# Performance work log

Measured on AMD Instinct MI355X. Metric: run time of the kernel, lower is better.

## Reference

```python
import jax, jax.numpy as jnp
import numpy as np

O, T, DIN, H, DOUT = 50000, 500000, 128, 256, 128


def setup_inputs() -> dict:
    key = jax.random.key(0)
    ks = jax.random.split(key, 12)
    s = 0.05
    return {
        "obj_vecs": jax.random.normal(ks[0], (O, DIN), jnp.float32),
        "pred_vecs": jax.random.normal(ks[1], (T, DIN), jnp.float32),
        "edges": jax.random.randint(ks[2], (T, 2), 0, O, jnp.int64),
        "w1a": jax.random.normal(ks[3], (3 * DIN, H), jnp.float32) * s,
        "b1a": jax.random.normal(ks[4], (H,), jnp.float32) * s,
        "w1b": jax.random.normal(ks[5], (H, 2 * H + DOUT), jnp.float32) * s,
        "b1b": jax.random.normal(ks[6], (2 * H + DOUT,), jnp.float32) * s,
        "w2a": jax.random.normal(ks[7], (H, H), jnp.float32) * s,
        "b2a": jax.random.normal(ks[8], (H,), jnp.float32) * s,
        "w2b": jax.random.normal(ks[9], (H, DOUT), jnp.float32) * s,
        "b2b": jax.random.normal(ks[10], (DOUT,), jnp.float32) * s,
    }


def reference(obj_vecs, pred_vecs, edges, w1a, b1a, w1b, b1b, w2a, b2a, w2b, b2b):
    n_obj = obj_vecs.shape[0]
    h_dim = w2a.shape[0]
    d_out = w2b.shape[1]
    s_idx = edges[:, 0]
    o_idx = edges[:, 1]
    # gather subject/object node features, concat with predicate: [T, 3*Din]
    cur_t = jnp.concatenate([obj_vecs[s_idx], pred_vecs, obj_vecs[o_idx]], axis=1)
    # edge MLP (net1): Linear-ReLU-Linear-ReLU -> [T, 2H + Dout]
    new_t = jax.nn.relu(jax.nn.relu(cur_t @ w1a + b1a) @ w1b + b1b)
    new_s = new_t[:, :h_dim]
    new_p = new_t[:, h_dim:h_dim + d_out]
    new_o = new_t[:, h_dim + d_out:]
    # scatter-add pooling back to nodes, both endpoints
    idx = jnp.concatenate([s_idx, o_idx])
    vals = jnp.concatenate([new_s, new_o], axis=0)
    pooled = jax.ops.segment_sum(vals, idx, num_segments=n_obj)
    # avg pooling: divide by per-node incidence count (clamped to >= 1)
    counts = jax.ops.segment_sum(jnp.ones(idx.shape[0], obj_vecs.dtype), idx,
                                 num_segments=n_obj)
    pooled = pooled / jnp.clip(counts, 1.0)[:, None]
    # node MLP (net2)
    new_obj = jax.nn.relu(jax.nn.relu(pooled @ w2a + b2a) @ w2b + b2b)
    return new_obj, new_p
```

## Files before the change

kernel.cpp:

```cpp
#include <hip/hip_runtime.h>


using f32x4 = __attribute__((ext_vector_type(4))) float;
using s16x8 = __attribute__((ext_vector_type(8))) short;
typedef unsigned short u16x8 __attribute__((ext_vector_type(8)));

static __device__ __forceinline__ unsigned short f2b(float f) {
    unsigned int u = __float_as_uint(f);
    unsigned int r = (u + 0x7fffu + ((u >> 16) & 1u)) >> 16;
    return (unsigned short)r;
}

static __device__ __forceinline__ float b2f(unsigned short b) {
    return __uint_as_float(((unsigned)b) << 16);
}

static __device__ __forceinline__ unsigned swz(unsigned row, unsigned byteoff) {
    return byteoff ^ ((row & 7u) << 4);
}

static __device__ __forceinline__ void gload_lds16(const unsigned short* g, unsigned short* l) {
    __builtin_amdgcn_global_load_lds(
        (const __attribute__((address_space(1))) unsigned int*)g,
        (__attribute__((address_space(3))) unsigned int*)l,
        16, 0, 0);
}

__global__ void prep_weights(const float* __restrict__ w1a, const float* __restrict__ w1b,
                             const float* __restrict__ w2a, const float* __restrict__ w2b,
                             unsigned short* __restrict__ w1aT, unsigned short* __restrict__ w1bT,
                             unsigned short* __restrict__ w2aT, unsigned short* __restrict__ w2bT) {
    int t = blockIdx.x * blockDim.x + threadIdx.x;
    if (t < 6 * 16384) {
        int kt = t >> 14;
        int rem = t & 16383; int c = rem >> 6, kk = rem & 63;
        unsigned byte = ((unsigned)(c * 128 + kk * 2)) ^ ((c & 7u) << 4);
        *(unsigned short*)((char*)w1aT + (size_t)kt * 32768 + byte) =
            f2b(w1a[(size_t)(kt * 64 + kk) * 256 + c]);
        return;
    }
    t -= 98304;
    if (t < 10 * 16384) {
        int tile = t >> 14; int nc = tile >> 1, kh = tile & 1;
        int rem = t & 16383; int c = rem >> 7, kk = rem & 127;
        unsigned byte = ((unsigned)(c * 256 + kk * 2)) ^ ((c & 7u) << 4);
        *(unsigned short*)((char*)w1bT + (size_t)tile * 32768 + byte) =
            f2b(w1b[(size_t)(kh * 128 + kk) * 640 + nc * 128 + c]);
        return;
    }
    t -= 163840;
    if (t < 65536) { int n = t >> 8, k = t & 255; w2aT[t] = f2b(w2a[k * 256 + n]); return; }
    t -= 65536;
    if (t < 32768) { int n = t >> 8, k = t & 255; w2bT[t] = f2b(w2b[k * 128 + n]); return; }
}

__global__ void count_kernel_i(const int* __restrict__ edges, int* __restrict__ cnt, int T) {
    int e = blockIdx.x * blockDim.x + threadIdx.x;
    if (e < T) {
        atomicAdd(&cnt[edges[2 * (long long)e]], 1);
        atomicAdd(&cnt[edges[2 * (long long)e + 1]], 1);
    }
}

__global__ void scan_kernel(const int* __restrict__ cnt, int* __restrict__ rowptr,
                            int* __restrict__ cursor, int O) {
    __shared__ int sc[1024];
    const int tid = threadIdx.x;
    const int per = (O + 1023) >> 10;
    const int base = tid * per;
    int s = 0;
    for (int i = 0; i < per; ++i) { int j = base + i; if (j < O) s += cnt[j]; }
    sc[tid] = s;
    __syncthreads();
    for (int d = 1; d < 1024; d <<= 1) {
        int v = (tid >= d) ? sc[tid - d] : 0;
        __syncthreads();
        sc[tid] += v;
        __syncthreads();
    }
    int off = sc[tid] - s;
    for (int i = 0; i < per; ++i) {
        int j = base + i;
        if (j < O) { rowptr[j] = off; cursor[j] = off; off += cnt[j]; }
    }
    if (tid == 0) rowptr[O] = sc[1023];
}

__global__ void fill_kernel(const int* __restrict__ edges, int* __restrict__ cursor,
                            int* __restrict__ csr, int T) {
    int e = blockIdx.x * blockDim.x + threadIdx.x;
    if (e < T) {
        int s = edges[2 * (long long)e];
        int o = edges[2 * (long long)e + 1];
        int ps = atomicAdd(&cursor[s], 1); csr[ps] = e;
        int po = atomicAdd(&cursor[o], 1); csr[po] = T + e;
    }
}

__global__ __launch_bounds__(512, 2) void edge_mlp(
    const float* __restrict__ obj, const float* __restrict__ pred,
    const int* __restrict__ edges,
    const unsigned short* __restrict__ w1aT, const float* __restrict__ b1a,
    const unsigned short* __restrict__ w1bT, const float* __restrict__ b1b,
    unsigned short* __restrict__ edgeout, float* __restrict__ outP, int T) {
    const int m0 = blockIdx.x * 128;
    const int tid = threadIdx.x;
    const int lane = tid & 63, wid = tid >> 6;
    const int wm = wid >> 2, wn = wid & 3;
    const bool evenL = ((lane & 1) == 0);

    __shared__ unsigned short U[65536];
    char* const ldsb = (char*)U;
    unsigned short* const abuf0 = (unsigned short*)(ldsb);
    unsigned short* const abuf1 = (unsigned short*)(ldsb + 16384);
    unsigned short* const Hbuf  = (unsigned short*)(ldsb);
    unsigned short* const bbuf0 = (unsigned short*)(ldsb + 65536);
    unsigned short* const bbuf1 = (unsigned short*)(ldsb + 98304);

    bool okR[4][4];
    #pragma unroll
    for (int mi = 0; mi < 4; ++mi)
        #pragma unroll
        for (int rr = 0; rr < 4; ++rr)
            okR[mi][rr] = (m0 + wm * 64 + mi * 16 + ((lane >> 4) << 2) + rr) < T;

    const int r = tid >> 2;
    const int q = tid & 3;
    int e_r = m0 + r; if (e_r >= T) e_r = T - 1;
    const int sIdx_r = edges[2 * (long long)e_r];
    const int oIdx_r = edges[2 * (long long)e_r + 1];

    auto aSrc = [&](int kt) -> const float4* {
        const float* s;
        if (kt < 2)      s = obj  + (long long)sIdx_r * 128 + kt * 64;
        else if (kt < 4) s = pred + (long long)e_r   * 128 + (kt - 2) * 64;
        else             s = obj  + (long long)oIdx_r * 128 + (kt - 4) * 64;
        return (const float4*)s;
    };

    auto stageB = [&](const unsigned short* gt, unsigned short* bb) {
        #pragma unroll
        for (int rr4 = 0; rr4 < 4; ++rr4) {
            unsigned off = wid * 4096u + rr4 * 1024u;
            gload_lds16((const unsigned short*)((const char*)gt + off + lane * 16u),
                        (unsigned short*)((char*)bb + off));
        }
    };

    auto writeA = [&](const float4* ap, unsigned short* ab) {
        #pragma unroll
        for (int i = 0; i < 4; ++i) {
            float4 v = ap[i];
            ushort4 pk; pk.x = f2b(v.x); pk.y = f2b(v.y); pk.z = f2b(v.z); pk.w = f2b(v.w);
            unsigned byte = (r * 128u + q * 32u + i * 8u) ^ ((r & 7u) << 4);
            *(ushort4*)((char*)ab + byte) = pk;
        }
    };

    f32x4 acc1[4][4];
    #pragma unroll
    for (int a = 0; a < 4; ++a)
        #pragma unroll
        for (int b = 0; b < 4; ++b) acc1[a][b] = f32x4{0.f, 0.f, 0.f, 0.f};

    auto mfma1 = [&](const unsigned short* ab, const unsigned short* bb) {
        #pragma unroll
        for (int ks = 0; ks < 2; ++ks) {
            const unsigned kk = ks * 32u + ((lane >> 4) << 3);
            s16x8 af[4];
            #pragma unroll
            for (int mi = 0; mi < 4; ++mi) {
                unsigned row = wm * 64u + mi * 16u + (lane & 15);
                af[mi] = *(const s16x8*)((const char*)ab + ((row * 128u + kk * 2u) ^ ((row & 7u) << 4)));
            }
            #pragma unroll
            for (int nj = 0; nj < 4; ++nj) {
                unsigned c = wn * 64u + nj * 16u + (lane & 15);
                s16x8 bf = *(const s16x8*)((const char*)bb + ((c * 128u + kk * 2u) ^ ((c & 7u) << 4)));
                #pragma unroll
                for (int mi = 0; mi < 4; ++mi)
                    acc1[mi][nj] = __builtin_amdgcn_mfma_f32_16x16x32_bf16(af[mi], bf, acc1[mi][nj], 0, 0, 0);
            }
        }
    };

    float4 ap[4];
    {
        const float4* s4 = aSrc(0);
        #pragma unroll
        for (int i = 0; i < 4; ++i) ap[i] = s4[q * 4 + i];
    }
    stageB(w1aT, bbuf0);
    writeA(ap, abuf0);
    __syncthreads();

    #pragma unroll
    for (int kt = 0; kt < 6; ++kt) {
        if (kt < 5) {
            const float4* s4 = aSrc(kt + 1);
            #pragma unroll
            for (int i = 0; i < 4; ++i) ap[i] = s4[q * 4 + i];
            stageB(w1aT + (size_t)(kt + 1) * 16384, ((kt + 1) & 1) ? bbuf1 : bbuf0);
        }
        mfma1((kt & 1) ? abuf1 : abuf0, (kt & 1) ? bbuf1 : bbuf0);
        if (kt < 5) writeA(ap, ((kt + 1) & 1) ? abuf1 : abuf0);
        __syncthreads();
    }

    stageB(w1bT, bbuf0);
    #pragma unroll
    for (int nj = 0; nj < 4; ++nj) {
        int col = wn * 64 + nj * 16 + (lane & 15);
        float bias = b1a[col];
        #pragma unroll
        for (int mi = 0; mi < 4; ++mi)
            #pragma unroll
            for (int rr = 0; rr < 4; ++rr) {
                unsigned row = wm * 64u + mi * 16u + ((lane >> 4) << 2) + rr;
                float v = acc1[mi][nj][rr] + bias;
                v = v > 0.f ? v : 0.f;
                *(unsigned short*)((char*)Hbuf + swz(row, row * 512u + col * 2u)) = f2b(v);
            }
    }
    __syncthreads();

    #pragma unroll
    for (int nc = 0; nc < 5; ++nc) {
        f32x4 acc2[4][2];
        #pragma unroll
        for (int a = 0; a < 4; ++a)
            #pragma unroll
            for (int b = 0; b < 2; ++b) acc2[a][b] = f32x4{0.f, 0.f, 0.f, 0.f};

        #pragma unroll
        for (int kh = 0; kh < 2; ++kh) {
            const int t10 = nc * 2 + kh;
            if (t10 < 9) stageB(w1bT + (size_t)(t10 + 1) * 16384, ((t10 + 1) & 1) ? bbuf1 : bbuf0);
            const unsigned short* bb = (t10 & 1) ? bbuf1 : bbuf0;
            #pragma unroll
            for (int ks = 0; ks < 4; ++ks) {
                const unsigned kkB = ks * 32u + ((lane >> 4) << 3);
                const unsigned kkH = kh * 128u + kkB;
                s16x8 af[4];
                #pragma unroll
                for (int mi = 0; mi < 4; ++mi) {
                    unsigned row = wm * 64u + mi * 16u + (lane & 15);
                    af[mi] = *(const s16x8*)((const char*)Hbuf + swz(row, row * 512u + kkH * 2u));
                }
                #pragma unroll
                for (int nj = 0; nj < 2; ++nj) {
                    unsigned c = wn * 32u + nj * 16u + (lane & 15);
                    s16x8 bf = *(const s16x8*)((const char*)bb + ((c * 256u + kkB * 2u) ^ ((c & 7u) << 4)));
                    #pragma unroll
                    for (int mi = 0; mi < 4; ++mi)
                        acc2[mi][nj] = __builtin_amdgcn_mfma_f32_16x16x32_bf16(af[mi], bf, acc2[mi][nj], 0, 0, 0);
                }
            }
            __syncthreads();
        }

        if (nc == 2) {
            #pragma unroll
            for (int nj = 0; nj < 2; ++nj) {
                int col = nc * 128 + wn * 32 + nj * 16 + (lane & 15);
                float bias = b1b[col];
                #pragma unroll
                for (int mi = 0; mi < 4; ++mi)
                    #pragma unroll
                    for (int rr = 0; rr < 4; ++rr) {
                        int row = wm * 64 + mi * 16 + ((lane >> 4) << 2) + rr;
                        if (okR[mi][rr]) {
                            float v = acc2[mi][nj][rr] + bias;
                            v = v > 0.f ? v : 0.f;
                            outP[(long long)(m0 + row) * 128 + (col - 256)] = v;
                        }
                    }
            }
        } else {
            #pragma unroll
            for (int nj = 0; nj < 2; ++nj) {
                int col = nc * 128 + wn * 32 + nj * 16 + (lane & 15);
                float bias = b1b[col];
                int pc = (nc < 2) ? col : (col - 384);
                int pcb = (lane & 1) ? (pc - 1) : pc;
                #pragma unroll
                for (int mi = 0; mi < 4; ++mi) {
                    float vv[4];
                    #pragma unroll
                    for (int rr = 0; rr < 4; ++rr) {
                        float v = acc2[mi][nj][rr] + bias;
                        vv[rr] = v > 0.f ? v : 0.f;
                    }
                    float nb0 = __shfl_xor(vv[0], 1);
                    float nb1 = __shfl_xor(vv[1], 1);
                    float nb2 = __shfl_xor(vv[2], 1);
                    float nb3 = __shfl_xor(vv[3], 1);
                    #pragma unroll
                    for (int k = 0; k < 2; ++k) {
                        float lo = evenL ? (k ? vv[1] : vv[0]) : (k ? nb3 : nb2);
                        float hi = evenL ? (k ? nb1 : nb0) : (k ? vv[3] : vv[2]);
                        int rsel = evenL ? k : 2 + k;
                        if (okR[mi][rsel]) {
                            int row = wm * 64 + mi * 16 + ((lane >> 4) << 2) + rsel;
                            size_t e = (size_t)(m0 + row);
                            size_t rid = (nc < 2) ? e : (size_t)T + e;
                            unsigned pk = ((unsigned)f2b(hi) << 16) | f2b(lo);
                            *(unsigned*)(edgeout + rid * 256 + pcb) = pk;
                        }
                    }
                }
            }
        }
    }
}

__global__ __launch_bounds__(256, 4) void pool_gather(
    const unsigned short* __restrict__ edgeout, const int* __restrict__ rowptr,
    const int* __restrict__ csr, unsigned short* __restrict__ pooled, int O) {
    int w = blockIdx.x * 4 + (threadIdx.x >> 6);
    if (w >= O) return;
    const int lane = threadIdx.x & 63;
    const int beg = rowptr[w], end = rowptr[w + 1];
    float ax = 0.f, ay = 0.f, az = 0.f, aw = 0.f;
    float bx = 0.f, by = 0.f, bz = 0.f, bw = 0.f;
    int i = beg;
    for (; i + 1 < end; i += 2) {
        int r0 = csr[i], r1 = csr[i + 1];
        ushort4 v0 = *(const ushort4*)(edgeout + (size_t)r0 * 256 + lane * 4);
        ushort4 v1 = *(const ushort4*)(edgeout + (size_t)r1 * 256 + lane * 4);
        ax += b2f(v0.x); ay += b2f(v0.y); az += b2f(v0.z); aw += b2f(v0.w);
        bx += b2f(v1.x); by += b2f(v1.y); bz += b2f(v1.z); bw += b2f(v1.w);
    }
    if (i < end) {
        int r0 = csr[i];
        ushort4 v0 = *(const ushort4*)(edgeout + (size_t)r0 * 256 + lane * 4);
        ax += b2f(v0.x); ay += b2f(v0.y); az += b2f(v0.z); aw += b2f(v0.w);
    }
    float inv = 1.f / fmaxf((float)(end - beg), 1.f);
    ushort4 o4;
    o4.x = f2b((ax + bx) * inv); o4.y = f2b((ay + by) * inv);
    o4.z = f2b((az + bz) * inv); o4.w = f2b((aw + bw) * inv);
    *(ushort4*)(pooled + (size_t)w * 256 + lane * 4) = o4;
}

__global__ __launch_bounds__(256, 2) void obj_mlp(
    const unsigned short* __restrict__ pooled,
    const unsigned short* __restrict__ w2aT, const float* __restrict__ b2a,
    const unsigned short* __restrict__ w2bT, const float* __restrict__ b2b,
    float* __restrict__ outObj, int O) {
    const int m0 = blockIdx.x * 64;
    const int tid = threadIdx.x;
    const int lane = tid & 63, wid = tid >> 6;
    const int wm = wid >> 1, wn = wid & 1;

    __shared__ unsigned short Abuf[64 * 256];

    {
        const int r = tid >> 2, q = tid & 3;
        int objc = m0 + r; if (objc >= O) objc = O - 1;
        const u16x8* s8 = (const u16x8*)(pooled + (size_t)objc * 256);
        #pragma unroll
        for (int i = 0; i < 8; ++i) {
            u16x8 v = s8[q * 8 + i];
            unsigned byte = r * 512u + (q * 64u + i * 8u) * 2u;
            *(u16x8*)((char*)Abuf + swz(r, byte)) = v;
        }
    }
    __syncthreads();

    f32x4 acc1[2][2][4];
    #pragma unroll
    for (int a = 0; a < 2; ++a)
        #pragma unroll
        for (int b = 0; b < 2; ++b)
            #pragma unroll
            for (int c = 0; c < 4; ++c) acc1[a][b][c] = f32x4{0.f, 0.f, 0.f, 0.f};
    #pragma unroll
    for (int ks = 0; ks < 8; ++ks) {
        const int klane = ks * 32 + ((lane >> 4) << 3);
        s16x8 af[2];
        #pragma unroll
        for (int mi = 0; mi < 2; ++mi) {
            int row = wm * 32 + mi * 16 + (lane & 15);
            af[mi] = *(const s16x8*)((const char*)Abuf + swz(row, row * 512u + klane * 2u));
        }
        #pragma unroll
        for (int nb = 0; nb < 2; ++nb)
            #pragma unroll
            for (int nj = 0; nj < 4; ++nj) {
                int col = nb * 128 + wn * 64 + nj * 16 + (lane & 15);
                s16x8 bf = *(const s16x8*)(w2aT + (long long)col * 256 + klane);
                #pragma unroll
                for (int mi = 0; mi < 2; ++mi)
                    acc1[nb][mi][nj] = __builtin_amdgcn_mfma_f32_16x16x32_bf16(af[mi], bf, acc1[nb][mi][nj], 0, 0, 0);
            }
    }
    __syncthreads();

    #pragma unroll
    for (int nb = 0; nb < 2; ++nb)
        #pragma unroll
        for (int nj = 0; nj < 4; ++nj) {
            int col = nb * 128 + wn * 64 + nj * 16 + (lane & 15);
            float bias = b2a[col];
            #pragma unroll
            for (int mi = 0; mi < 2; ++mi)
                #pragma unroll
                for (int rr = 0; rr < 4; ++rr) {
                    int row = wm * 32 + mi * 16 + ((lane >> 4) << 2) + rr;
                    float v = acc1[nb][mi][nj][rr] + bias;
                    v = v > 0.f ? v : 0.f;
                    *(unsigned short*)((char*)Abuf + swz(row, row * 512u + col * 2u)) = f2b(v);
                }
        }
    __syncthreads();

    f32x4 acc2[2][4];
    #pragma unroll
    for (int b = 0; b < 2; ++b)
        #pragma unroll
        for (int c = 0; c < 4; ++c) acc2[b][c] = f32x4{0.f, 0.f, 0.f, 0.f};
    #pragma unroll
    for (int ks = 0; ks < 8; ++ks) {
        const int klane = ks * 32 + ((lane >> 4) << 3);
        s16x8 af[2];
        #pragma unroll
        for (int mi = 0; mi < 2; ++mi) {
            int row = wm * 32 + mi * 16 + (lane & 15);
            af[mi] = *(const s16x8*)((const char*)Abuf + swz(row, row * 512u + klane * 2u));
        }
        #pragma unroll
        for (int nj = 0; nj < 4; ++nj) {
            int col = wn * 64 + nj * 16 + (lane & 15);
            s16x8 bf = *(const s16x8*)(w2bT + (long long)col * 256 + klane);
            #pragma unroll
            for (int mi = 0; mi < 2; ++mi)
                acc2[mi][nj] = __builtin_amdgcn_mfma_f32_16x16x32_bf16(af[mi], bf, acc2[mi][nj], 0, 0, 0);
        }
    }

    #pragma unroll
    for (int nj = 0; nj < 4; ++nj) {
        int col = wn * 64 + nj * 16 + (lane & 15);
        float bias = b2b[col];
        #pragma unroll
        for (int mi = 0; mi < 2; ++mi)
            #pragma unroll
            for (int rr = 0; rr < 4; ++rr) {
                int row = wm * 32 + mi * 16 + ((lane >> 4) << 2) + rr;
                int o = m0 + row;
                if (o < O) {
                    float v = acc2[mi][nj][rr] + bias;
                    v = v > 0.f ? v : 0.f;
                    outObj[(long long)o * 128 + col] = v;
                }
            }
    }
}

extern "C" void kernel_launch(void* const* d_in, const int* in_sizes, int n_in,
                              void* d_out, int out_size, void* d_ws, size_t ws_size,
                              hipStream_t stream) {
    const float* obj  = (const float*)d_in[0];
    const float* pred = (const float*)d_in[1];
    const int*   edges = (const int*)d_in[2];
    const float* w1a = (const float*)d_in[3];
    const float* b1a = (const float*)d_in[4];
    const float* w1b = (const float*)d_in[5];
    const float* b1b = (const float*)d_in[6];
    const float* w2a = (const float*)d_in[7];
    const float* b2a = (const float*)d_in[8];
    const float* w2b = (const float*)d_in[9];
    const float* b2b = (const float*)d_in[10];

    const int O = in_sizes[0] / 128;
    const int T = in_sizes[1] / 128;

    auto al = [](size_t x) { return (x + 255) & ~(size_t)255; };
    const size_t szEdgeout = (size_t)2 * T * 256 * 2;
    const size_t szPooled  = (size_t)O * 256 * 2;
    const size_t szCnt     = (size_t)O * 4;
    const size_t szRow     = (size_t)(O + 1) * 4;
    const size_t szCsr     = (size_t)2 * T * 4;

    size_t off = 0;
    char* ws = (char*)d_ws;
    unsigned short* edgeout = (unsigned short*)(ws + off); off += al(szEdgeout);
    unsigned short* pooled  = (unsigned short*)(ws + off); off += al(szPooled);
    int* cnt    = (int*)(ws + off); off += al(szCnt);
    int* cursor = (int*)(ws + off); off += al(szCnt);
    int* rowptr = (int*)(ws + off); off += al(szRow);
    int* csr    = (int*)(ws + off); off += al(szCsr);
    unsigned short* w1aT = (unsigned short*)(ws + off); off += (size_t)6 * 16384 * 2;
    unsigned short* w1bT = (unsigned short*)(ws + off); off += (size_t)10 * 16384 * 2;
    unsigned short* w2aT = (unsigned short*)(ws + off); off += (size_t)256 * 256 * 2;
    unsigned short* w2bT = (unsigned short*)(ws + off);

    float* outObj = (float*)d_out;
    float* outP   = (float*)d_out + (size_t)O * 128;

    hipMemsetAsync(cnt, 0, szCnt, stream);
    const int prepElems = 98304 + 163840 + 65536 + 32768;
    prep_weights<<<(prepElems + 255) / 256, 256, 0, stream>>>(w1a, w1b, w2a, w2b, w1aT, w1bT, w2aT, w2bT);
    count_kernel_i<<<(T + 255) / 256, 256, 0, stream>>>(edges, cnt, T);
    scan_kernel<<<1, 1024, 0, stream>>>(cnt, rowptr, cursor, O);
    fill_kernel<<<(T + 255) / 256, 256, 0, stream>>>(edges, cursor, csr, T);
    edge_mlp<<<(T + 127) / 128, 512, 0, stream>>>(obj, pred, edges, w1aT, b1a, w1bT, b1b, edgeout, outP, T);
    pool_gather<<<(O + 3) / 4, 256, 0, stream>>>(edgeout, rowptr, csr, pooled, O);
    obj_mlp<<<(O + 63) / 64, 256, 0, stream>>>(pooled, w2aT, b2a, w2bT, b2b, outObj, O);
}
```

Before: 1.003 ms.

## Replace syncthreads with fine-grained waitcnt barriers and deepen prefetch in edge MLP

Replaces __syncthreads in the fused edge MLP with explicit vmcnt/lgkmcnt waits and raw barriers. A-tile gathers are now issued two stages ahead, and the first w1b tile is prefetched during the last GEMM1 step. It also preloads biases into registers, raises wave priority around MFMA sections, and unrolls the pooling gather by four to keep more loads in flight. Hand-tuned vmcnt counts must match the compiler's actual outstanding memory ops; if they do not, this risks races or correctness bugs.

```diff
diff --git a/kernel.cpp b/kernel.cpp
--- a/kernel.cpp
+++ b/kernel.cpp
@@ -4,6 +4,14 @@
 using f32x4 = __attribute__((ext_vector_type(4))) float;
 using s16x8 = __attribute__((ext_vector_type(8))) short;
 typedef unsigned short u16x8 __attribute__((ext_vector_type(8)));
+
+#define VMCNT0  asm volatile("s_waitcnt vmcnt(0)" ::: "memory")
+#define VMCNT4  asm volatile("s_waitcnt vmcnt(4)" ::: "memory")
+#define VMCNT16 asm volatile("s_waitcnt vmcnt(16)" ::: "memory")
+#define VMCNT32 asm volatile("s_waitcnt vmcnt(32)" ::: "memory")
+#define LGKM0   asm volatile("s_waitcnt lgkmcnt(0)" ::: "memory")
+#define BAR     __builtin_amdgcn_s_barrier()
+#define SCHEDB  __builtin_amdgcn_sched_barrier(0)
 
 static __device__ __forceinline__ unsigned short f2b(float f) {
     unsigned int u = __float_as_uint(f);
@@ -130,6 +138,15 @@
     const int sIdx_r = edges[2 * (long long)e_r];
     const int oIdx_r = edges[2 * (long long)e_r + 1];
 
+    float bias1[4], bias2[5][2];
+    #pragma unroll
+    for (int nj = 0; nj < 4; ++nj) bias1[nj] = b1a[wn * 64 + nj * 16 + (lane & 15)];
+    #pragma unroll
+    for (int nc = 0; nc < 5; ++nc)
+        #pragma unroll
+        for (int nj = 0; nj < 2; ++nj)
+            bias2[nc][nj] = b1b[nc * 128 + wn * 32 + nj * 16 + (lane & 15)];
+
     auto aSrc = [&](int kt) -> const float4* {
         const float* s;
         if (kt < 2)      s = obj  + (long long)sIdx_r * 128 + kt * 64;
@@ -190,39 +207,58 @@
         #pragma unroll
         for (int i = 0; i < 4; ++i) ap[i] = s4[q * 4 + i];
     }
+    writeA(ap, abuf0);
     stageB(w1aT, bbuf0);
-    writeA(ap, abuf0);
-    __syncthreads();
+    {
+        const float4* s4 = aSrc(1);
+        #pragma unroll
+        for (int i = 0; i < 4; ++i) ap[i] = s4[q * 4 + i];
+    }
+    VMCNT4;
+    LGKM0;
+    BAR; SCHEDB;
 
     #pragma unroll
     for (int kt = 0; kt < 6; ++kt) {
+        if (kt < 5) stageB(w1aT + (size_t)(kt + 1) * 16384, ((kt + 1) & 1) ? bbuf1 : bbuf0);
+        else        stageB(w1bT, bbuf0);
+        __builtin_amdgcn_s_setprio(1);
+        mfma1((kt & 1) ? abuf1 : abuf0, (kt & 1) ? bbuf1 : bbuf0);
+        __builtin_amdgcn_s_setprio(0);
         if (kt < 5) {
-            const float4* s4 = aSrc(kt + 1);
-            #pragma unroll
-            for (int i = 0; i < 4; ++i) ap[i] = s4[q * 4 + i];
-            stageB(w1aT + (size_t)(kt + 1) * 16384, ((kt + 1) & 1) ? bbuf1 : bbuf0);
-        }
-        mfma1((kt & 1) ? abuf1 : abuf0, (kt & 1) ? bbuf1 : bbuf0);
-        if (kt < 5) writeA(ap, ((kt + 1) & 1) ? abuf1 : abuf0);
-        __syncthreads();
-    }
-
-    stageB(w1bT, bbuf0);
+            VMCNT4;
+            writeA(ap, ((kt + 1) & 1) ? abuf1 : abuf0);
+            if (kt < 4) {
+                const float4* s4 = aSrc(kt + 2);
+                #pragma unroll
+                for (int i = 0; i < 4; ++i) ap[i] = s4[q * 4 + i];
+                VMCNT4;
+            } else {
+                VMCNT0;
+            }
+            LGKM0;
+            BAR; SCHEDB;
+        }
+    }
+
+    LGKM0;
+    BAR; SCHEDB;
     #pragma unroll
     for (int nj = 0; nj < 4; ++nj) {
-        int col = wn * 64 + nj * 16 + (lane & 15);
-        float bias = b1a[col];
         #pragma unroll
         for (int mi = 0; mi < 4; ++mi)
             #pragma unroll
             for (int rr = 0; rr < 4; ++rr) {
                 unsigned row = wm * 64u + mi * 16u + ((lane >> 4) << 2) + rr;
-                float v = acc1[mi][nj][rr] + bias;
+                unsigned col = wn * 64u + nj * 16u + (lane & 15);
+                float v = acc1[mi][nj][rr] + bias1[nj];
                 v = v > 0.f ? v : 0.f;
                 *(unsigned short*)((char*)Hbuf + swz(row, row * 512u + col * 2u)) = f2b(v);
             }
     }
-    __syncthreads();
+    LGKM0;
+    VMCNT0;
+    BAR; SCHEDB;
 
     #pragma unroll
     for (int nc = 0; nc < 5; ++nc) {
@@ -237,6 +273,7 @@
             const int t10 = nc * 2 + kh;
             if (t10 < 9) stageB(w1bT + (size_t)(t10 + 1) * 16384, ((t10 + 1) & 1) ? bbuf1 : bbuf0);
             const unsigned short* bb = (t10 & 1) ? bbuf1 : bbuf0;
+            __builtin_amdgcn_s_setprio(1);
             #pragma unroll
             for (int ks = 0; ks < 4; ++ks) {
                 const unsigned kkB = ks * 32u + ((lane >> 4) << 3);
@@ -256,31 +293,36 @@
                         acc2[mi][nj] = __builtin_amdgcn_mfma_f32_16x16x32_bf16(af[mi], bf, acc2[mi][nj], 0, 0, 0);
                 }
             }
-            __syncthreads();
+            __builtin_amdgcn_s_setprio(0);
+
+            if (kh == 0) {
+                VMCNT0;
+                BAR; SCHEDB;
+            }
         }
 
         if (nc == 2) {
             #pragma unroll
             for (int nj = 0; nj < 2; ++nj) {
                 int col = nc * 128 + wn * 32 + nj * 16 + (lane & 15);
-                float bias = b1b[col];
                 #pragma unroll
                 for (int mi = 0; mi < 4; ++mi)
                     #pragma unroll
                     for (int rr = 0; rr < 4; ++rr) {
                         int row = wm * 64 + mi * 16 + ((lane >> 4) << 2) + rr;
                         if (okR[mi][rr]) {
-                            float v = acc2[mi][nj][rr] + bias;
+                            float v = acc2[mi][nj][rr] + bias2[nc][nj];
                             v = v > 0.f ? v : 0.f;
                             outP[(long long)(m0 + row) * 128 + (col - 256)] = v;
                         }
                     }
             }
+            VMCNT32;
+            BAR; SCHEDB;
         } else {
             #pragma unroll
             for (int nj = 0; nj < 2; ++nj) {
                 int col = nc * 128 + wn * 32 + nj * 16 + (lane & 15);
-                float bias = b1b[col];
                 int pc = (nc < 2) ? col : (col - 384);
                 int pcb = (lane & 1) ? (pc - 1) : pc;
                 #pragma unroll
@@ -288,7 +330,7 @@
                     float vv[4];
                     #pragma unroll
                     for (int rr = 0; rr < 4; ++rr) {
-                        float v = acc2[mi][nj][rr] + bias;
+                        float v = acc2[mi][nj][rr] + bias2[nc][nj];
                         vv[rr] = v > 0.f ? v : 0.f;
                     }
                     float nb0 = __shfl_xor(vv[0], 1);
@@ -310,6 +352,10 @@
                     }
                 }
             }
+            if (nc < 4) {
+                VMCNT16;
+                BAR; SCHEDB;
+            }
         }
     }
 }
@@ -324,14 +370,18 @@
     float ax = 0.f, ay = 0.f, az = 0.f, aw = 0.f;
     float bx = 0.f, by = 0.f, bz = 0.f, bw = 0.f;
     int i = beg;
-    for (; i + 1 < end; i += 2) {
-        int r0 = csr[i], r1 = csr[i + 1];
+    for (; i + 3 < end; i += 4) {
+        int r0 = csr[i], r1 = csr[i + 1], r2 = csr[i + 2], r3 = csr[i + 3];
         ushort4 v0 = *(const ushort4*)(edgeout + (size_t)r0 * 256 + lane * 4);
         ushort4 v1 = *(const ushort4*)(edgeout + (size_t)r1 * 256 + lane * 4);
+        ushort4 v2 = *(const ushort4*)(edgeout + (size_t)r2 * 256 + lane * 4);
+        ushort4 v3 = *(const ushort4*)(edgeout + (size_t)r3 * 256 + lane * 4);
         ax += b2f(v0.x); ay += b2f(v0.y); az += b2f(v0.z); aw += b2f(v0.w);
         bx += b2f(v1.x); by += b2f(v1.y); bz += b2f(v1.z); bw += b2f(v1.w);
-    }
-    if (i < end) {
+        ax += b2f(v2.x); ay += b2f(v2.y); az += b2f(v2.z); aw += b2f(v2.w);
+        bx += b2f(v3.x); by += b2f(v3.y); bz += b2f(v3.z); bw += b2f(v3.w);
+    }
+    for (; i < end; ++i) {
         int r0 = csr[i];
         ushort4 v0 = *(const ushort4*)(edgeout + (size_t)r0 * 256 + lane * 4);
         ax += b2f(v0.x); ay += b2f(v0.y); az += b2f(v0.z); aw += b2f(v0.w);
```

Measured after the change: 930.7 us. 7.2% less time.

## Load edge-MLP weights directly into registers in MFMA fragment order, shrink edge tile

Applied to the files above, without the earlier changes.

Weights w1a/w1b are now pre-permuted into per-lane MFMA fragment order, so edge_mlp reads B operands straight from global/L2 into registers with double-buffered prefetch instead of staging them through LDS. The edge tile drops to 64 rows with 256 threads, the whole 64x384 A tile is gathered into LDS up front, and fewer barriers are needed, aiming at higher occupancy (3 blocks per CU). The trade-off is that every wave re-reads its weight fragments from cache with no LDS sharing across blocks. pool_gather is also unrolled to four gathers in flight.

```diff
diff --git a/kernel.cpp b/kernel.cpp
--- a/kernel.cpp
+++ b/kernel.cpp
@@ -19,33 +19,31 @@
     return byteoff ^ ((row & 7u) << 4);
 }
 
-static __device__ __forceinline__ void gload_lds16(const unsigned short* g, unsigned short* l) {
-    __builtin_amdgcn_global_load_lds(
-        (const __attribute__((address_space(1))) unsigned int*)g,
-        (__attribute__((address_space(3))) unsigned int*)l,
-        16, 0, 0);
-}
-
 __global__ void prep_weights(const float* __restrict__ w1a, const float* __restrict__ w1b,
                              const float* __restrict__ w2a, const float* __restrict__ w2b,
-                             unsigned short* __restrict__ w1aT, unsigned short* __restrict__ w1bT,
+                             unsigned short* __restrict__ w1aF, unsigned short* __restrict__ w1bF,
                              unsigned short* __restrict__ w2aT, unsigned short* __restrict__ w2bT) {
     int t = blockIdx.x * blockDim.x + threadIdx.x;
-    if (t < 6 * 16384) {
-        int kt = t >> 14;
-        int rem = t & 16383; int c = rem >> 6, kk = rem & 63;
-        unsigned byte = ((unsigned)(c * 128 + kk * 2)) ^ ((c & 7u) << 4);
-        *(unsigned short*)((char*)w1aT + (size_t)kt * 32768 + byte) =
-            f2b(w1a[(size_t)(kt * 64 + kk) * 256 + c]);
+    if (t < 98304) {
+        int j = t & 7; int f = t >> 3;
+        int lane = f & 63; int rest = f >> 6;
+        int ks = rest % 12; int rest2 = rest / 12;
+        int nj = rest2 & 3; int wn = rest2 >> 2;
+        int c = wn * 64 + nj * 16 + (lane & 15);
+        int k = ks * 32 + ((lane >> 4) << 3) + j;
+        w1aF[t] = f2b(w1a[(size_t)k * 256 + c]);
         return;
     }
     t -= 98304;
-    if (t < 10 * 16384) {
-        int tile = t >> 14; int nc = tile >> 1, kh = tile & 1;
-        int rem = t & 16383; int c = rem >> 7, kk = rem & 127;
-        unsigned byte = ((unsigned)(c * 256 + kk * 2)) ^ ((c & 7u) << 4);
-        *(unsigned short*)((char*)w1bT + (size_t)tile * 32768 + byte) =
-            f2b(w1b[(size_t)(kh * 128 + kk) * 640 + nc * 128 + c]);
+    if (t < 163840) {
+        int j = t & 7; int f = t >> 3;
+        int lane = f & 63; int rest = f >> 6;
+        int ks = rest & 7; rest >>= 3;
+        int nj = rest & 1; rest >>= 1;
+        int wn = rest & 3; int nc = rest >> 2;
+        int c = nc * 128 + wn * 32 + nj * 16 + (lane & 15);
+        int k = ks * 32 + ((lane >> 4) << 3) + j;
+        w1bF[t] = f2b(w1b[(size_t)k * 640 + c]);
         return;
     }
     t -= 163840;
@@ -97,65 +95,57 @@
     }
 }
 
-__global__ __launch_bounds__(512, 2) void edge_mlp(
+__global__ __launch_bounds__(256, 3) void edge_mlp(
     const float* __restrict__ obj, const float* __restrict__ pred,
     const int* __restrict__ edges,
-    const unsigned short* __restrict__ w1aT, const float* __restrict__ b1a,
-    const unsigned short* __restrict__ w1bT, const float* __restrict__ b1b,
+    const unsigned short* __restrict__ w1aF, const float* __restrict__ b1a,
+    const unsigned short* __restrict__ w1bF, const float* __restrict__ b1b,
     unsigned short* __restrict__ edgeout, float* __restrict__ outP, int T) {
-    const int m0 = blockIdx.x * 128;
+    const int m0 = blockIdx.x * 64;
     const int tid = threadIdx.x;
-    const int lane = tid & 63, wid = tid >> 6;
-    const int wm = wid >> 2, wn = wid & 3;
+    const int lane = tid & 63;
+    const int wn = tid >> 6;
     const bool evenL = ((lane & 1) == 0);
 
-    __shared__ unsigned short U[65536];
-    char* const ldsb = (char*)U;
-    unsigned short* const abuf0 = (unsigned short*)(ldsb);
-    unsigned short* const abuf1 = (unsigned short*)(ldsb + 16384);
-    unsigned short* const Hbuf  = (unsigned short*)(ldsb);
-    unsigned short* const bbuf0 = (unsigned short*)(ldsb + 65536);
-    unsigned short* const bbuf1 = (unsigned short*)(ldsb + 98304);
+    __shared__ unsigned short A[24576];
+    char* const ldsb = (char*)A;
 
     bool okR[4][4];
     #pragma unroll
     for (int mi = 0; mi < 4; ++mi)
         #pragma unroll
         for (int rr = 0; rr < 4; ++rr)
-            okR[mi][rr] = (m0 + wm * 64 + mi * 16 + ((lane >> 4) << 2) + rr) < T;
-
-    const int r = tid >> 2;
-    const int q = tid & 3;
-    int e_r = m0 + r; if (e_r >= T) e_r = T - 1;
-    const int sIdx_r = edges[2 * (long long)e_r];
-    const int oIdx_r = edges[2 * (long long)e_r + 1];
-
-    auto aSrc = [&](int kt) -> const float4* {
-        const float* s;
-        if (kt < 2)      s = obj  + (long long)sIdx_r * 128 + kt * 64;
-        else if (kt < 4) s = pred + (long long)e_r   * 128 + (kt - 2) * 64;
-        else             s = obj  + (long long)oIdx_r * 128 + (kt - 4) * 64;
-        return (const float4*)s;
-    };
-
-    auto stageB = [&](const unsigned short* gt, unsigned short* bb) {
-        #pragma unroll
-        for (int rr4 = 0; rr4 < 4; ++rr4) {
-            unsigned off = wid * 4096u + rr4 * 1024u;
-            gload_lds16((const unsigned short*)((const char*)gt + off + lane * 16u),
-                        (unsigned short*)((char*)bb + off));
-        }
-    };
-
-    auto writeA = [&](const float4* ap, unsigned short* ab) {
-        #pragma unroll
-        for (int i = 0; i < 4; ++i) {
-            float4 v = ap[i];
-            ushort4 pk; pk.x = f2b(v.x); pk.y = f2b(v.y); pk.z = f2b(v.z); pk.w = f2b(v.w);
-            unsigned byte = (r * 128u + q * 32u + i * 8u) ^ ((r & 7u) << 4);
-            *(ushort4*)((char*)ab + byte) = pk;
-        }
-    };
+            okR[mi][rr] = (m0 + mi * 16 + ((lane >> 4) << 2) + rr) < T;
+
+    {
+        const int r = tid >> 2, q = tid & 3;
+        int e_r = m0 + r; if (e_r >= T) e_r = T - 1;
+        const float* srcs[3];
+        srcs[0] = obj  + (long long)edges[2 * (long long)e_r] * 128;
+        srcs[1] = pred + (long long)e_r * 128;
+        srcs[2] = obj  + (long long)edges[2 * (long long)e_r + 1] * 128;
+        #pragma unroll
+        for (int src = 0; src < 3; ++src) {
+            const float4* s4 = (const float4*)(srcs[src] + q * 32);
+            #pragma unroll
+            for (int i = 0; i < 8; ++i) {
+                float4 v = s4[i];
+                ushort4 pk; pk.x = f2b(v.x); pk.y = f2b(v.y); pk.z = f2b(v.z); pk.w = f2b(v.w);
+                unsigned byte = (r * 768u + (src * 128u + q * 32u + i * 4u) * 2u) ^ ((r & 7u) << 4);
+                *(ushort4*)(ldsb + byte) = pk;
+            }
+        }
+    }
+    __syncthreads();
+
+    float bias1[4], bias2[5][2];
+    #pragma unroll
+    for (int nj = 0; nj < 4; ++nj) bias1[nj] = b1a[wn * 64 + nj * 16 + (lane & 15)];
+    #pragma unroll
+    for (int nc = 0; nc < 5; ++nc)
+        #pragma unroll
+        for (int nj = 0; nj < 2; ++nj)
+            bias2[nc][nj] = b1b[nc * 128 + wn * 32 + nj * 16 + (lane & 15)];
 
     f32x4 acc1[4][4];
     #pragma unroll
@@ -163,63 +153,46 @@
         #pragma unroll
         for (int b = 0; b < 4; ++b) acc1[a][b] = f32x4{0.f, 0.f, 0.f, 0.f};
 
-    auto mfma1 = [&](const unsigned short* ab, const unsigned short* bb) {
-        #pragma unroll
-        for (int ks = 0; ks < 2; ++ks) {
+    {
+        const s16x8* fb = (const s16x8*)(w1aF) + (size_t)wn * 4 * 12 * 64 + lane;
+        s16x8 bf[2][4];
+        #pragma unroll
+        for (int nj = 0; nj < 4; ++nj) bf[0][nj] = fb[(nj * 12 + 0) * 64];
+        #pragma unroll
+        for (int ks = 0; ks < 12; ++ks) {
+            if (ks < 11) {
+                #pragma unroll
+                for (int nj = 0; nj < 4; ++nj)
+                    bf[(ks + 1) & 1][nj] = fb[(nj * 12 + ks + 1) * 64];
+            }
             const unsigned kk = ks * 32u + ((lane >> 4) << 3);
             s16x8 af[4];
             #pragma unroll
             for (int mi = 0; mi < 4; ++mi) {
-                unsigned row = wm * 64u + mi * 16u + (lane & 15);
-                af[mi] = *(const s16x8*)((const char*)ab + ((row * 128u + kk * 2u) ^ ((row & 7u) << 4)));
-            }
-            #pragma unroll
-            for (int nj = 0; nj < 4; ++nj) {
-                unsigned c = wn * 64u + nj * 16u + (lane & 15);
-                s16x8 bf = *(const s16x8*)((const char*)bb + ((c * 128u + kk * 2u) ^ ((c & 7u) << 4)));
+                unsigned row = mi * 16u + (lane & 15);
+                af[mi] = *(const s16x8*)(ldsb + ((row * 768u + kk * 2u) ^ ((row & 7u) << 4)));
+            }
+            #pragma unroll
+            for (int nj = 0; nj < 4; ++nj)
                 #pragma unroll
                 for (int mi = 0; mi < 4; ++mi)
-                    acc1[mi][nj] = __builtin_amdgcn_mfma_f32_16x16x32_bf16(af[mi], bf, acc1[mi][nj], 0, 0, 0);
-            }
-        }
-    };
-
-    float4 ap[4];
-    {
-        const float4* s4 = aSrc(0);
-        #pragma unroll
-        for (int i = 0; i < 4; ++i) ap[i] = s4[q * 4 + i];
-    }
-    stageB(w1aT, bbuf0);
-    writeA(ap, abuf0);
-    __syncthreads();
-
-    #pragma unroll
-    for (int kt = 0; kt < 6; ++kt) {
-        if (kt < 5) {
-            const float4* s4 = aSrc(kt + 1);
-            #pragma unroll
-            for (int i = 0; i < 4; ++i) ap[i] = s4[q * 4 + i];
-            stageB(w1aT + (size_t)(kt + 1) * 16384, ((kt + 1) & 1) ? bbuf1 : bbuf0);
-        }
-        mfma1((kt & 1) ? abuf1 : abuf0, (kt & 1) ? bbuf1 : bbuf0);
-        if (kt < 5) writeA(ap, ((kt + 1) & 1) ? abuf1 : abuf0);
-        __syncthreads();
-    }
-
-    stageB(w1bT, bbuf0);
+                    acc1[mi][nj] = __builtin_amdgcn_mfma_f32_16x16x32_bf16(af[mi], bf[ks & 1][nj], acc1[mi][nj], 0, 0, 0);
+        }
+    }
+
+    __syncthreads();
+
     #pragma unroll
     for (int nj = 0; nj < 4; ++nj) {
-        int col = wn * 64 + nj * 16 + (lane & 15);
-        float bias = b1a[col];
+        unsigned col = wn * 64u + nj * 16u + (lane & 15);
         #pragma unroll
         for (int mi = 0; mi < 4; ++mi)
             #pragma unroll
             for (int rr = 0; rr < 4; ++rr) {
-                unsigned row = wm * 64u + mi * 16u + ((lane >> 4) << 2) + rr;
-                float v = acc1[mi][nj][rr] + bias;
+                unsigned row = mi * 16u + ((lane >> 4) << 2) + rr;
+                float v = acc1[mi][nj][rr] + bias1[nj];
                 v = v > 0.f ? v : 0.f;
-                *(unsigned short*)((char*)Hbuf + swz(row, row * 512u + col * 2u)) = f2b(v);
+                *(unsigned short*)(ldsb + ((row * 512u + col * 2u) ^ ((row & 7u) << 4))) = f2b(v);
             }
     }
     __syncthreads();
@@ -232,45 +205,42 @@
             #pragma unroll
             for (int b = 0; b < 2; ++b) acc2[a][b] = f32x4{0.f, 0.f, 0.f, 0.f};
 
-        #pragma unroll
-        for (int kh = 0; kh < 2; ++kh) {
-            const int t10 = nc * 2 + kh;
-            if (t10 < 9) stageB(w1bT + (size_t)(t10 + 1) * 16384, ((t10 + 1) & 1) ? bbuf1 : bbuf0);
-            const unsigned short* bb = (t10 & 1) ? bbuf1 : bbuf0;
-            #pragma unroll
-            for (int ks = 0; ks < 4; ++ks) {
-                const unsigned kkB = ks * 32u + ((lane >> 4) << 3);
-                const unsigned kkH = kh * 128u + kkB;
-                s16x8 af[4];
-                #pragma unroll
-                for (int mi = 0; mi < 4; ++mi) {
-                    unsigned row = wm * 64u + mi * 16u + (lane & 15);
-                    af[mi] = *(const s16x8*)((const char*)Hbuf + swz(row, row * 512u + kkH * 2u));
-                }
-                #pragma unroll
-                for (int nj = 0; nj < 2; ++nj) {
-                    unsigned c = wn * 32u + nj * 16u + (lane & 15);
-                    s16x8 bf = *(const s16x8*)((const char*)bb + ((c * 256u + kkB * 2u) ^ ((c & 7u) << 4)));
-                    #pragma unroll
-                    for (int mi = 0; mi < 4; ++mi)
-                        acc2[mi][nj] = __builtin_amdgcn_mfma_f32_16x16x32_bf16(af[mi], bf, acc2[mi][nj], 0, 0, 0);
-                }
-            }
-            __syncthreads();
+        const s16x8* fb = (const s16x8*)(w1bF) + ((size_t)(nc * 4 + wn) * 2 * 8) * 64 + lane;
+        s16x8 bf[2][2];
+        #pragma unroll
+        for (int nj = 0; nj < 2; ++nj) bf[0][nj] = fb[(nj * 8 + 0) * 64];
+        #pragma unroll
+        for (int ks = 0; ks < 8; ++ks) {
+            if (ks < 7) {
+                #pragma unroll
+                for (int nj = 0; nj < 2; ++nj)
+                    bf[(ks + 1) & 1][nj] = fb[(nj * 8 + ks + 1) * 64];
+            }
+            const unsigned kk = ks * 32u + ((lane >> 4) << 3);
+            s16x8 af[4];
+            #pragma unroll
+            for (int mi = 0; mi < 4; ++mi) {
+                unsigned row = mi * 16u + (lane & 15);
+                af[mi] = *(const s16x8*)(ldsb + ((row * 512u + kk * 2u) ^ ((row & 7u) << 4)));
+            }
+            #pragma unroll
+            for (int nj = 0; nj < 2; ++nj)
+                #pragma unroll
+                for (int mi = 0; mi < 4; ++mi)
+                    acc2[mi][nj] = __builtin_amdgcn_mfma_f32_16x16x32_bf16(af[mi], bf[ks & 1][nj], acc2[mi][nj], 0, 0, 0);
         }
 
         if (nc == 2) {
             #pragma unroll
             for (int nj = 0; nj < 2; ++nj) {
                 int col = nc * 128 + wn * 32 + nj * 16 + (lane & 15);
-                float bias = b1b[col];
                 #pragma unroll
                 for (int mi = 0; mi < 4; ++mi)
                     #pragma unroll
                     for (int rr = 0; rr < 4; ++rr) {
-                        int row = wm * 64 + mi * 16 + ((lane >> 4) << 2) + rr;
+                        int row = mi * 16 + ((lane >> 4) << 2) + rr;
                         if (okR[mi][rr]) {
-                            float v = acc2[mi][nj][rr] + bias;
+                            float v = acc2[mi][nj][rr] + bias2[nc][nj];
                             v = v > 0.f ? v : 0.f;
                             outP[(long long)(m0 + row) * 128 + (col - 256)] = v;
                         }
@@ -280,7 +250,6 @@
             #pragma unroll
             for (int nj = 0; nj < 2; ++nj) {
                 int col = nc * 128 + wn * 32 + nj * 16 + (lane & 15);
-                float bias = b1b[col];
                 int pc = (nc < 2) ? col : (col - 384);
                 int pcb = (lane & 1) ? (pc - 1) : pc;
                 #pragma unroll
@@ -288,7 +257,7 @@
                     float vv[4];
                     #pragma unroll
                     for (int rr = 0; rr < 4; ++rr) {
-                        float v = acc2[mi][nj][rr] + bias;
+                        float v = acc2[mi][nj][rr] + bias2[nc][nj];
                         vv[rr] = v > 0.f ? v : 0.f;
                     }
                     float nb0 = __shfl_xor(vv[0], 1);
@@ -301,7 +270,7 @@
                         float hi = evenL ? (k ? nb1 : nb0) : (k ? vv[3] : vv[2]);
                         int rsel = evenL ? k : 2 + k;
                         if (okR[mi][rsel]) {
-                            int row = wm * 64 + mi * 16 + ((lane >> 4) << 2) + rsel;
+                            int row = mi * 16 + ((lane >> 4) << 2) + rsel;
                             size_t e = (size_t)(m0 + row);
                             size_t rid = (nc < 2) ? e : (size_t)T + e;
                             unsigned pk = ((unsigned)f2b(hi) << 16) | f2b(lo);
@@ -324,14 +293,18 @@
     float ax = 0.f, ay = 0.f, az = 0.f, aw = 0.f;
     float bx = 0.f, by = 0.f, bz = 0.f, bw = 0.f;
     int i = beg;
-    for (; i + 1 < end; i += 2) {
-        int r0 = csr[i], r1 = csr[i + 1];
+    for (; i + 3 < end; i += 4) {
+        int r0 = csr[i], r1 = csr[i + 1], r2 = csr[i + 2], r3 = csr[i + 3];
         ushort4 v0 = *(const ushort4*)(edgeout + (size_t)r0 * 256 + lane * 4);
         ushort4 v1 = *(const ushort4*)(edgeout + (size_t)r1 * 256 + lane * 4);
+        ushort4 v2 = *(const ushort4*)(edgeout + (size_t)r2 * 256 + lane * 4);
+        ushort4 v3 = *(const ushort4*)(edgeout + (size_t)r3 * 256 + lane * 4);
         ax += b2f(v0.x); ay += b2f(v0.y); az += b2f(v0.z); aw += b2f(v0.w);
         bx += b2f(v1.x); by += b2f(v1.y); bz += b2f(v1.z); bw += b2f(v1.w);
-    }
-    if (i < end) {
+        ax += b2f(v2.x); ay += b2f(v2.y); az += b2f(v2.z); aw += b2f(v2.w);
+        bx += b2f(v3.x); by += b2f(v3.y); bz += b2f(v3.z); bw += b2f(v3.w);
+    }
+    for (; i < end; ++i) {
         int r0 = csr[i];
         ushort4 v0 = *(const ushort4*)(edgeout + (size_t)r0 * 256 + lane * 4);
         ax += b2f(v0.x); ay += b2f(v0.y); az += b2f(v0.z); aw += b2f(v0.w);
@@ -491,8 +464,8 @@
     int* cursor = (int*)(ws + off); off += al(szCnt);
     int* rowptr = (int*)(ws + off); off += al(szRow);
     int* csr    = (int*)(ws + off); off += al(szCsr);
-    unsigned short* w1aT = (unsigned short*)(ws + off); off += (size_t)6 * 16384 * 2;
-    unsigned short* w1bT = (unsigned short*)(ws + off); off += (size_t)10 * 16384 * 2;
+    unsigned short* w1aF = (unsigned short*)(ws + off); off += (size_t)98304 * 2;
+    unsigned short* w1bF = (unsigned short*)(ws + off); off += (size_t)163840 * 2;
     unsigned short* w2aT = (unsigned short*)(ws + off); off += (size_t)256 * 256 * 2;
     unsigned short* w2bT = (unsigned short*)(ws + off);
 
@@ -501,11 +474,11 @@
 
     hipMemsetAsync(cnt, 0, szCnt, stream);
     const int prepElems = 98304 + 163840 + 65536 + 32768;
-    prep_weights<<<(prepElems + 255) / 256, 256, 0, stream>>>(w1a, w1b, w2a, w2b, w1aT, w1bT, w2aT, w2bT);
+    prep_weights<<<(prepElems + 255) / 256, 256, 0, stream>>>(w1a, w1b, w2a, w2b, w1aF, w1bF, w2aT, w2bT);
     count_kernel_i<<<(T + 255) / 256, 256, 0, stream>>>(edges, cnt, T);
     scan_kernel<<<1, 1024, 0, stream>>>(cnt, rowptr, cursor, O);
     fill_kernel<<<(T + 255) / 256, 256, 0, stream>>>(edges, cursor, csr, T);
-    edge_mlp<<<(T + 127) / 128, 512, 0, stream>>>(obj, pred, edges, w1aT, b1a, w1bT, b1b, edgeout, outP, T);
+    edge_mlp<<<(T + 63) / 64, 256, 0, stream>>>(obj, pred, edges, w1aF, b1a, w1bF, b1b, edgeout, outP, T);
     pool_gather<<<(O + 3) / 4, 256, 0, stream>>>(edgeout, rowptr, csr, pooled, O);
     obj_mlp<<<(O + 63) / 64, 256, 0, stream>>>(pooled, w2aT, b2a, w2bT, b2b, outObj, O);
 }
```

Result: slower. 1.901 ms (+89.6%).
